# Kernel optimization log

Measured on AMD Instinct MI355X. Metric: run time of the kernel, lower is better.

Reference implementation:

```python
import jax, jax.numpy as jnp
import numpy as np

N = 4_194_304
B = 64
H = 16
TAU = 1.0


def setup_inputs() -> dict:
    key = jax.random.key(0)
    ks = jax.random.split(key, 8)
    pos = jax.random.normal(ks[0], (N, 3), dtype=jnp.float32)
    reflectance = jax.random.uniform(ks[1], (N,), dtype=jnp.float32)
    batch = jnp.sort(jax.random.randint(ks[2], (N,), 0, B).astype(jnp.int32))
    gumbels = jax.random.gumbel(ks[3], (B, 2), dtype=jnp.float32)
    W1 = jax.random.normal(ks[4], (4, H), dtype=jnp.float32) * 0.5
    b1 = jnp.zeros((H,), dtype=jnp.float32)
    W2 = jax.random.normal(ks[5], (H, H), dtype=jnp.float32) * 0.25
    b2 = jnp.zeros((H,), dtype=jnp.float32)
    Wg = jax.random.normal(ks[6], (H, 2), dtype=jnp.float32) * 0.25
    bg = jnp.array([0.0, 2.0], dtype=jnp.float32)  # gate_nn bias init per module
    return {"pos": pos, "reflectance": reflectance, "batch": batch, "gumbels": gumbels,
            "W1": W1, "b1": b1, "W2": W2, "b2": b2, "Wg": Wg, "bg": bg}


def reference(pos, reflectance, batch, gumbels, W1, b1, W2, b2, Wg, bg):
    # point-wise MLP: [N,4] -> [N,H]
    features = jnp.concatenate([pos, reflectance[:, None]], axis=-1)
    h = jax.nn.relu(features @ W1 + b1)
    h = jax.nn.relu(h @ W2 + b2)
    # batch-indexed max pool: [N,H] -> [B,H]
    sample_features = jax.ops.segment_max(h, batch, num_segments=B)
    gate_logits = sample_features @ Wg + bg  # [B,2]
    # gumbel-softmax (hard=False as in forward)
    gate_decision = jax.nn.softmax((gate_logits + gumbels) / TAU, axis=-1)
    # gather per-point gate and scale reflectance
    use_reflectance = gate_decision[:, 1][batch]  # [N]
    return use_reflectance * reflectance
```

## Files before the change

### kernel.cpp

```cpp
#include <hip/hip_runtime.h>
#include <hip/hip_bf16.h>


#define N_PTS 4194304
#define NB 64
#define NH 16
#define WPB 4
#define ITERS 16
#define PTW (64 * ITERS)
#define PPB (WPB * PTW)
#define NBLK (N_PTS / PPB)
#define NENT (NBLK * 2)

typedef __attribute__((ext_vector_type(8))) short bf16x8;
typedef __attribute__((ext_vector_type(4))) float f32x4;
union U8 { bf16x8 v; unsigned u[4]; unsigned short s[8]; };

struct Rec { int idA, idB, bpos; };

__device__ __forceinline__ unsigned pk2(float a, float b) {
    float2 t; t.x = a; t.y = b;
    __hip_bfloat162 r = __float22bfloat162_rn(t);
    unsigned u;
    __builtin_memcpy(&u, &r, sizeof(u));
    return u;
}
__device__ __forceinline__ unsigned short f2bf(float x) {
    unsigned u = __float_as_uint(x);
    u = u + 0x7fffu + ((u >> 16) & 1u);
    return (unsigned short)(u >> 16);
}

__global__ __launch_bounds__(256) void mlp_segmax_kernel(
    const float* __restrict__ pos,
    const float* __restrict__ refl,
    const int*   __restrict__ batch,
    const float* __restrict__ W1, const float* __restrict__ b1,
    const float* __restrict__ W2, const float* __restrict__ b2,
    float* __restrict__ pv,
    int*   __restrict__ pid,
    Rec*   __restrict__ recs)
{
    __shared__ float lv[WPB][2][NH];
    __shared__ int   li[WPB][2];
    __shared__ int   lbp[WPB];

    const int lane = threadIdx.x & 63;
    const int wid  = threadIdx.x >> 6;
    const int col  = lane & 15;
    const int g    = lane >> 4;
    const int wb   = (blockIdx.x * WPB + wid) * PTW;

    U8 A1, A2;
#pragma unroll
    for (int e = 0; e < 4; ++e) {
        A1.s[e]     = f2bf(W1[e * NH + col]);
        A1.s[e + 4] = 0;
        A2.s[e]     = f2bf(W2[(4 * g + e) * NH + col]);
        A2.s[e + 4] = 0;
    }
    f32x4 c1, c2;
#pragma unroll
    for (int r = 0; r < 4; ++r) { c1[r] = b1[4 * g + r]; c2[r] = b2[4 * g + r]; }

    const int idA = batch[wb];
    const int idB = batch[wb + PTW - 1];

    f32x4 accA = {0.f, 0.f, 0.f, 0.f};
    f32x4 accB = {0.f, 0.f, 0.f, 0.f};
    int bposw = 0x7fffffff;

    if (idA == idB) {
#pragma unroll 2
        for (int it = 0; it < ITERS; ++it) {
            const int idx = wb + it * 64 + lane;
            const float x = pos[idx * 3 + 0];
            const float y = pos[idx * 3 + 1];
            const float z = pos[idx * 3 + 2];
            const float w = refl[idx];
            const unsigned F01 = pk2(x, y), F23 = pk2(z, w);
#pragma unroll
            for (int t = 0; t < 4; ++t) {
                const bool mine = (g == t);
                U8 B;
                B.u[0] = mine ? F01 : 0u;
                B.u[1] = mine ? F23 : 0u;
                B.u[2] = 0u; B.u[3] = 0u;
                f32x4 d = __builtin_amdgcn_mfma_f32_16x16x32_bf16(A1.v, B.v, c1, 0, 0, 0);
                U8 P;
                P.u[0] = pk2(fmaxf(d[0], 0.f), fmaxf(d[1], 0.f));
                P.u[1] = pk2(fmaxf(d[2], 0.f), fmaxf(d[3], 0.f));
                P.u[2] = 0u; P.u[3] = 0u;
                f32x4 h = __builtin_amdgcn_mfma_f32_16x16x32_bf16(A2.v, P.v, c2, 0, 0, 0);
#pragma unroll
                for (int r = 0; r < 4; ++r) accA[r] = fmaxf(accA[r], h[r]);
            }
        }
    } else {
        for (int it = 0; it < ITERS; ++it) {
            const int idx = wb + it * 64 + lane;
            const unsigned long long mk = __ballot(batch[idx] != idA);
            if (mk) bposw = min(bposw, wb + it * 64 + (__ffsll((long long)mk) - 1));
        }
#pragma unroll 2
        for (int it = 0; it < ITERS; ++it) {
            const int base = wb + it * 64;
            const int idx  = base + lane;
            const float x = pos[idx * 3 + 0];
            const float y = pos[idx * 3 + 1];
            const float z = pos[idx * 3 + 2];
            const float w = refl[idx];
            const unsigned F01 = pk2(x, y), F23 = pk2(z, w);
#pragma unroll
            for (int t = 0; t < 4; ++t) {
                const bool mine = (g == t);
                U8 B;
                B.u[0] = mine ? F01 : 0u;
                B.u[1] = mine ? F23 : 0u;
                B.u[2] = 0u; B.u[3] = 0u;
                f32x4 d = __builtin_amdgcn_mfma_f32_16x16x32_bf16(A1.v, B.v, c1, 0, 0, 0);
                U8 P;
                P.u[0] = pk2(fmaxf(d[0], 0.f), fmaxf(d[1], 0.f));
                P.u[1] = pk2(fmaxf(d[2], 0.f), fmaxf(d[3], 0.f));
                P.u[2] = 0u; P.u[3] = 0u;
                f32x4 h = __builtin_amdgcn_mfma_f32_16x16x32_bf16(A2.v, P.v, c2, 0, 0, 0);
                const bool m = (base + t * 16 + col) < bposw;
#pragma unroll
                for (int r = 0; r < 4; ++r) {
                    accA[r] = fmaxf(accA[r], m ? h[r] : 0.f);
                    accB[r] = fmaxf(accB[r], m ? 0.f : h[r]);
                }
            }
        }
    }

#pragma unroll
    for (int mk = 1; mk <= 8; mk <<= 1) {
#pragma unroll
        for (int r = 0; r < 4; ++r) {
            accA[r] = fmaxf(accA[r], __shfl_xor(accA[r], mk));
            accB[r] = fmaxf(accB[r], __shfl_xor(accB[r], mk));
        }
    }
    if (col == 0) {
        *reinterpret_cast<float4*>(&lv[wid][0][4 * g]) =
            make_float4(accA[0], accA[1], accA[2], accA[3]);
        *reinterpret_cast<float4*>(&lv[wid][1][4 * g]) =
            make_float4(accB[0], accB[1], accB[2], accB[3]);
    }
    if (lane == 0) {
        li[wid][0] = idA; li[wid][1] = idB;
        lbp[wid]   = (idA != idB) ? bposw : 0x7fffffff;
    }
    __syncthreads();

    if (threadIdx.x < NH) {
        const int d   = threadIdx.x;
        const int ida = li[0][0];
        const int idb = li[WPB - 1][1];
        float mA = 0.f, mB = 0.f;
#pragma unroll
        for (int s = 0; s < WPB; ++s)
#pragma unroll
            for (int hh = 0; hh < 2; ++hh) {
                const float val = lv[s][hh][d];
                if (li[s][hh] == ida) mA = fmaxf(mA, val);
                else                  mB = fmaxf(mB, val);
            }
        pv[(blockIdx.x * 2 + 0) * NH + d] = mA;
        pv[(blockIdx.x * 2 + 1) * NH + d] = mB;
        if (d == 0) {
            pid[blockIdx.x * 2 + 0] = ida;
            pid[blockIdx.x * 2 + 1] = idb;
            int bp = 0x7fffffff;
#pragma unroll
            for (int s = 0; s < WPB; ++s) {
                if (li[s][0] != ida) bp = min(bp, (int)(blockIdx.x * PPB + s * PTW));
                else if (lbp[s] != 0x7fffffff) bp = min(bp, lbp[s]);
            }
            Rec r; r.idA = ida; r.idB = idb; r.bpos = bp;
            recs[blockIdx.x] = r;
        }
    }
}

__global__ __launch_bounds__(1024) void stage2_kernel(
    const float* __restrict__ pv, const int* __restrict__ pid,
    const float* __restrict__ Wg, const float* __restrict__ bg,
    const float* __restrict__ gum, float* __restrict__ gate)
{
    __shared__ unsigned int sm[NB * NH];
    const int tid = threadIdx.x;
    sm[tid] = 0u;
    __syncthreads();

#pragma unroll
    for (int i = tid; i < NENT * 4; i += 1024) {
        const float4 v = reinterpret_cast<const float4*>(pv)[i];
        const int e  = i >> 2;
        const int d0 = (i & 3) * 4;
        const int id = pid[e];
        atomicMax(&sm[id * NH + d0 + 0], __float_as_uint(v.x));
        atomicMax(&sm[id * NH + d0 + 1], __float_as_uint(v.y));
        atomicMax(&sm[id * NH + d0 + 2], __float_as_uint(v.z));
        atomicMax(&sm[id * NH + d0 + 3], __float_as_uint(v.w));
    }
    __syncthreads();

    if (tid < NB) {
        float l0 = bg[0] + gum[tid * 2 + 0];
        float l1 = bg[1] + gum[tid * 2 + 1];
#pragma unroll
        for (int k = 0; k < NH; ++k) {
            const float s = __uint_as_float(sm[tid * NH + k]);
            l0 = fmaf(s, Wg[k * 2 + 0], l0);
            l1 = fmaf(s, Wg[k * 2 + 1], l1);
        }
        gate[tid] = 1.f / (1.f + expf(-(l1 - l0)));
    }
}

__global__ __launch_bounds__(256) void scale_kernel(
    const float* __restrict__ refl,
    const Rec*   __restrict__ recs,
    const float* __restrict__ gate,
    float* __restrict__ out)
{
    const Rec rec = recs[blockIdx.x >> 2];
    const float gA = gate[rec.idA];
    const float gB = gate[rec.idB];

    const int p0 = (blockIdx.x * 256 + threadIdx.x) * 4;
    const float4 rr = *reinterpret_cast<const float4*>(refl + p0);
    float4 o;
    o.x = ((p0 + 0) < rec.bpos ? gA : gB) * rr.x;
    o.y = ((p0 + 1) < rec.bpos ? gA : gB) * rr.y;
    o.z = ((p0 + 2) < rec.bpos ? gA : gB) * rr.z;
    o.w = ((p0 + 3) < rec.bpos ? gA : gB) * rr.w;
    *reinterpret_cast<float4*>(out + p0) = o;
}

extern "C" void kernel_launch(void* const* d_in, const int* in_sizes, int n_in,
                              void* d_out, int out_size, void* d_ws, size_t ws_size,
                              hipStream_t stream) {
    const float* pos   = (const float*)d_in[0];
    const float* refl  = (const float*)d_in[1];
    const int*   batch = (const int*)d_in[2];
    const float* gumb  = (const float*)d_in[3];
    const float* W1    = (const float*)d_in[4];
    const float* b1    = (const float*)d_in[5];
    const float* W2    = (const float*)d_in[6];
    const float* b2    = (const float*)d_in[7];
    const float* Wg    = (const float*)d_in[8];
    const float* bg    = (const float*)d_in[9];
    float* out = (float*)d_out;

    float* pv   = (float*)d_ws;
    int*   pid  = (int*)((char*)d_ws + 131072);
    Rec*   recs = (Rec*)((char*)d_ws + 139264);
    float* gate = (float*)((char*)d_ws + 151552);

    mlp_segmax_kernel<<<NBLK, 256, 0, stream>>>(pos, refl, batch,
                                                W1, b1, W2, b2, pv, pid, recs);
    stage2_kernel<<<1, 1024, 0, stream>>>(pv, pid, Wg, bg, gumb, gate);
    scale_kernel<<<N_PTS / 1024, 256, 0, stream>>>(refl, recs, gate, out);
}
```

Before: 42.89 us.

## Stage point data through double-buffered LDS with vectorized float4 loads

The per-lane strided scalar loads of pos (stride 3) and reflectance are replaced by coalesced float4 global loads into a per-wave double-buffered shared-memory tile. The next tile is loaded into registers while the current one is processed by MFMA, then written to LDS. The two fast and slow code paths are merged into one loop with a runtime branch on the accumulation step. This trades uncoalesced stride-3 loads for LDS traffic, block-wide __syncthreads each stage, and 32KB of shared memory per block, which may reduce occupancy.

```diff
diff --git a/kernel.cpp b/kernel.cpp
--- a/kernel.cpp
+++ b/kernel.cpp
@@ -6,8 +6,8 @@
 #define NB 64
 #define NH 16
 #define WPB 4
-#define ITERS 16
-#define PTW (64 * ITERS)
+#define SITERS 4
+#define PTW (256 * SITERS)
 #define PPB (WPB * PTW)
 #define NBLK (N_PTS / PPB)
 #define NENT (NBLK * 2)
@@ -41,6 +41,7 @@
     int*   __restrict__ pid,
     Rec*   __restrict__ recs)
 {
+    __shared__ float sbuf[WPB][2][1024];
     __shared__ float lv[WPB][2][NH];
     __shared__ int   li[WPB][2];
     __shared__ int   lbp[WPB];
@@ -65,19 +66,46 @@
 
     const int idA = batch[wb];
     const int idB = batch[wb + PTW - 1];
+    const bool isSlow = (idA != idB);
+
+    int bposw = 0x7fffffff;
+    if (isSlow) {
+        for (int it = 0; it < PTW / 64; ++it) {
+            const int idx = wb + it * 64 + lane;
+            const unsigned long long mk = __ballot(batch[idx] != idA);
+            if (mk) bposw = min(bposw, wb + it * 64 + (__ffsll((long long)mk) - 1));
+        }
+    }
 
     f32x4 accA = {0.f, 0.f, 0.f, 0.f};
     f32x4 accB = {0.f, 0.f, 0.f, 0.f};
-    int bposw = 0x7fffffff;
-
-    if (idA == idB) {
-#pragma unroll 2
-        for (int it = 0; it < ITERS; ++it) {
-            const int idx = wb + it * 64 + lane;
-            const float x = pos[idx * 3 + 0];
-            const float y = pos[idx * 3 + 1];
-            const float z = pos[idx * 3 + 2];
-            const float w = refl[idx];
+
+    float4 t0, t1, t2, t3;
+#define LOADS(s)  do { \
+        const float4* gp = (const float4*)(pos + (size_t)(wb + (s) * 256) * 3); \
+        const float4* gr = (const float4*)(refl + wb + (s) * 256);              \
+        t0 = gp[0 * 64 + lane]; t1 = gp[1 * 64 + lane];                         \
+        t2 = gp[2 * 64 + lane]; t3 = gr[lane]; } while (0)
+#define WRITES(s) do { \
+        float4* lp = (float4*)&sbuf[wid][(s) & 1][0];                           \
+        lp[0 * 64 + lane] = t0; lp[1 * 64 + lane] = t1;                         \
+        lp[2 * 64 + lane] = t2; lp[3 * 64 + lane] = t3; } while (0)
+
+    LOADS(0);
+    WRITES(0);
+    __syncthreads();
+
+    for (int s = 0; s < SITERS; ++s) {
+        if (s + 1 < SITERS) LOADS(s + 1);
+        const float* lb = &sbuf[wid][s & 1][0];
+        const int    sb = wb + s * 256;
+#pragma unroll
+        for (int j = 0; j < 4; ++j) {
+            const int pl = j * 64 + lane;
+            const float x = lb[pl * 3 + 0];
+            const float y = lb[pl * 3 + 1];
+            const float z = lb[pl * 3 + 2];
+            const float w = lb[768 + pl];
             const unsigned F01 = pk2(x, y), F23 = pk2(z, w);
 #pragma unroll
             for (int t = 0; t < 4; ++t) {
@@ -92,47 +120,24 @@
                 P.u[1] = pk2(fmaxf(d[2], 0.f), fmaxf(d[3], 0.f));
                 P.u[2] = 0u; P.u[3] = 0u;
                 f32x4 h = __builtin_amdgcn_mfma_f32_16x16x32_bf16(A2.v, P.v, c2, 0, 0, 0);
-#pragma unroll
-                for (int r = 0; r < 4; ++r) accA[r] = fmaxf(accA[r], h[r]);
-            }
-        }
-    } else {
-        for (int it = 0; it < ITERS; ++it) {
-            const int idx = wb + it * 64 + lane;
-            const unsigned long long mk = __ballot(batch[idx] != idA);
-            if (mk) bposw = min(bposw, wb + it * 64 + (__ffsll((long long)mk) - 1));
-        }
-#pragma unroll 2
-        for (int it = 0; it < ITERS; ++it) {
-            const int base = wb + it * 64;
-            const int idx  = base + lane;
-            const float x = pos[idx * 3 + 0];
-            const float y = pos[idx * 3 + 1];
-            const float z = pos[idx * 3 + 2];
-            const float w = refl[idx];
-            const unsigned F01 = pk2(x, y), F23 = pk2(z, w);
-#pragma unroll
-            for (int t = 0; t < 4; ++t) {
-                const bool mine = (g == t);
-                U8 B;
-                B.u[0] = mine ? F01 : 0u;
-                B.u[1] = mine ? F23 : 0u;
-                B.u[2] = 0u; B.u[3] = 0u;
-                f32x4 d = __builtin_amdgcn_mfma_f32_16x16x32_bf16(A1.v, B.v, c1, 0, 0, 0);
-                U8 P;
-                P.u[0] = pk2(fmaxf(d[0], 0.f), fmaxf(d[1], 0.f));
-                P.u[1] = pk2(fmaxf(d[2], 0.f), fmaxf(d[3], 0.f));
-                P.u[2] = 0u; P.u[3] = 0u;
-                f32x4 h = __builtin_amdgcn_mfma_f32_16x16x32_bf16(A2.v, P.v, c2, 0, 0, 0);
-                const bool m = (base + t * 16 + col) < bposw;
-#pragma unroll
-                for (int r = 0; r < 4; ++r) {
-                    accA[r] = fmaxf(accA[r], m ? h[r] : 0.f);
-                    accB[r] = fmaxf(accB[r], m ? 0.f : h[r]);
+                if (!isSlow) {
+#pragma unroll
+                    for (int r = 0; r < 4; ++r) accA[r] = fmaxf(accA[r], h[r]);
+                } else {
+                    const bool m = (sb + j * 64 + t * 16 + col) < bposw;
+#pragma unroll
+                    for (int r = 0; r < 4; ++r) {
+                        accA[r] = fmaxf(accA[r], m ? h[r] : 0.f);
+                        accB[r] = fmaxf(accB[r], m ? 0.f : h[r]);
+                    }
                 }
             }
         }
-    }
+        if (s + 1 < SITERS) WRITES(s + 1);
+        __syncthreads();
+    }
+#undef LOADS
+#undef WRITES
 
 #pragma unroll
     for (int mk = 1; mk <= 8; mk <<= 1) {
@@ -150,7 +155,7 @@
     }
     if (lane == 0) {
         li[wid][0] = idA; li[wid][1] = idB;
-        lbp[wid]   = (idA != idB) ? bposw : 0x7fffffff;
+        lbp[wid]   = isSlow ? bposw : 0x7fffffff;
     }
     __syncthreads();
 
```

After: 55.16 us. 1.29x slower.
